# Kernel tuning notes

Hardware: AMD Instinct MI355X
Metric: run time of the kernel (lower is better)

The kernel has to match this reference:

```python
import jax, jax.numpy as jnp
import numpy as np

B, N, V = 1024, 256, 200


def setup_inputs() -> dict:
    key = jax.random.key(0)
    ks = jax.random.split(key, 24)
    merged = jax.random.normal(ks[0], (B, N, 15), dtype=jnp.float32)
    # active flag column in {0,1}; row 0 is the subject bus and is always active
    flag = (jax.random.uniform(ks[1], (B, N)) < 0.5).astype(jnp.float32)
    flag = flag.at[:, 0].set(1.0)
    merged = merged.at[:, :, 14].set(flag)
    a = jax.random.normal(ks[2], (B,), dtype=jnp.float32)
    w = lambda k, s: jax.random.normal(k, s, dtype=jnp.float32) * 0.05
    return dict(
        merged=merged, a=a,
        up_Wq=w(ks[3], (7, V)), up_Wk=w(ks[4], (14, V)), up_Wv=w(ks[5], (14, V)),
        dn_Wq=w(ks[6], (7, V)), dn_Wk=w(ks[7], (14, V)), dn_Wv=w(ks[8], (14, V)),
        pv_Wq=w(ks[9], (7, V)), pv_Wk=w(ks[10], (7, V)), pv_Wv=w(ks[11], (7, V)),
        t_W1=w(ks[12], (3, V, V)), t_b1=w(ks[13], (3, V)),
        t_W2=w(ks[14], (3, V, 1)), t_b2=w(ks[15], (3, 1)),
        e_W1=w(ks[16], (4, V)), e_b1=w(ks[17], (V,)),
        e_W2=w(ks[18], (V, V)), e_b2=w(ks[19], (V,)),
        e_W3=w(ks[20], (V, 1)), e_b3=w(ks[21], (1,)),
        gamma=jnp.ones((V,), jnp.float32), beta=jnp.zeros((V,), jnp.float32),
    )


def reference(merged, a, up_Wq, up_Wk, up_Wv, dn_Wq, dn_Wk, dn_Wv,
              pv_Wq, pv_Wk, pv_Wv, t_W1, t_b1, t_W2, t_b2,
              e_W1, e_b1, e_W2, e_b2, e_W3, e_b3, gamma, beta):
    v_dim = gamma.shape[0]
    scale = np.float32(1.0 / np.sqrt(v_dim))
    # merged_s[0, 6] = a  (subject bus action)
    merged = merged.at[:, 0, 6].set(a)
    # subtract subject bus id from id columns 0 and 7
    subj_id = merged[:, 0:1, 0]                       # [B,1]
    merged = merged.at[:, :, 0].add(-subj_id)
    merged = merged.at[:, :, 7].add(-subj_id)
    subj_loc = merged[:, 0:1, 2]                      # [B,1]
    flag = merged[:, :, 14]                           # [B,N]
    loc = merged[:, :, 2]                             # [B,N]
    up_mask = (loc < subj_loc) & (flag == 1.0)        # active upstream (excludes subject: loc==subj_loc)
    dn_mask = (loc > subj_loc) & (flag == 1.0)        # active downstream
    pv_mask = flag == 0.0                             # passive buses (row 0 is active by construction)
    ego = merged[:, 0, :7]                            # [B,7]
    f14 = merged[:, :, :14]                           # [B,N,14]
    f7 = merged[:, :, :7]                             # [B,N,7]

    def attend(Wq, Wk, Wv, feat, mask):
        # single-query cross attention: ego query vs ragged (masked) neighbor set
        q = ego @ Wq                                  # [B,V]
        k = jnp.einsum('bnf,fv->bnv', feat, Wk)
        v = jnp.einsum('bnf,fv->bnv', feat, Wv)
        s = jnp.einsum('bv,bnv->bn', q, k) * scale
        s = jnp.where(mask, s, jnp.float32(-1e9))
        out = jnp.einsum('bn,bnv->bv', jax.nn.softmax(s, axis=-1), v)
        # empty neighbor set -> zeros(v_dim) (compute_attention_target fallback)
        return jnp.where(mask.any(-1, keepdims=True), out, 0.0)

    u = attend(up_Wq, up_Wk, up_Wv, f14, up_mask)
    d = attend(dn_Wq, dn_Wk, dn_Wv, f14, dn_mask)
    p = attend(pv_Wq, pv_Wk, pv_Wv, f7, pv_mask)

    def bn(x):  # BatchNorm1d in training mode: batch statistics, biased var
        m = x.mean(0)
        var = x.var(0)
        return gamma * (x - m) * jax.lax.rsqrt(var + 1e-5) + beta

    t = jnp.stack([bn(u), bn(d), bn(p)], 0)           # [3,B,V]
    h = jax.nn.elu(jnp.einsum('kbv,kvw->kbw', t, t_W1) + t_b1[:, None, :])
    heads = jnp.einsum('kbw,kwo->kbo', h, t_W2) + t_b2[:, None, :]  # [3,B,1]
    ego_t = merged[:, 0, 3:7]                         # cols [3,4,5,6] = [hb,hf,occp,a]
    q1 = jax.nn.relu(ego_t @ e_W1 + e_b1)
    q1 = jax.nn.relu(q1 @ e_W2 + e_b2)
    Q1 = q1 @ e_W3 + e_b3                             # [B,1]
    G1 = Q1 + heads[0] + heads[1] + heads[2]
    return G1.reshape(-1, 1)
```

## Files before the change

kernel.cpp:

```cpp
#include <hip/hip_runtime.h>
#include <math.h>

#define BB 1024
#define NN 256
#define VV 200
#define BT 8
#define NSH 16

#define WS_M    0
#define WS_STAT 256
#define WS_X    19456

__global__ __launch_bounds__(256) void k_prep(const float* __restrict__ upWq, const float* __restrict__ upWk,
                                              const float* __restrict__ dnWq, const float* __restrict__ dnWk,
                                              const float* __restrict__ pvWq, const float* __restrict__ pvWk,
                                              float* __restrict__ ws, float* __restrict__ out) {
    __shared__ float wq[7 * VV];
    __shared__ float wk[14 * VV];
    int blk = blockIdx.x, tid = threadIdx.x;
    float* stat = ws + WS_STAT;
    for (int i = blk * 256 + tid; i < 2 * NSH * 600; i += 8 * 256) stat[i] = 0.f;
    for (int i = blk * 256 + tid; i < BB; i += 8 * 256) out[i] = 0.f;

    if (blk < 3) {
        const float* Wq = blk == 0 ? upWq : (blk == 1 ? dnWq : pvWq);
        const float* Wk = blk == 0 ? upWk : (blk == 1 ? dnWk : pvWk);
        int F = (blk == 2) ? 7 : 14;
        int off = blk == 0 ? 0 : (blk == 1 ? 98 : 196);
        for (int i = tid; i < 7 * VV; i += 256) wq[i] = Wq[i];
        for (int i = tid; i < F * VV; i += 256) wk[i] = Wk[i];
        __syncthreads();
        if (tid < 7 * F) {
            int i = tid / F, f = tid % F;
            float s = 0.f;
            for (int v = 0; v < VV; v++) s += wq[i * VV + v] * wk[f * VV + v];
            ws[WS_M + off + tid] = s;
        }
    }
}

__global__ __launch_bounds__(256) void k_attn(
    const float* __restrict__ merged, const float* __restrict__ a,
    const float* __restrict__ upWv, const float* __restrict__ dnWv, const float* __restrict__ pvWv,
    float* __restrict__ ws) {
    int b = blockIdx.x;
    int tid = threadIdx.x;
    int lane = tid & 63, wave = tid >> 6;

    __shared__ float sm[NN * 15];
    __shared__ float eMsh[35];
    __shared__ float psh[3 * NN];
    __shared__ float part[245];
    __shared__ float csh[35];
    __shared__ float wred[4][3];

    const float* gM = ws + WS_M;
    float* g_sum = ws + WS_STAT;
    float* g_ss  = ws + WS_STAT + NSH * 600;
    float* g_x   = ws + WS_X;

    const float4* g4 = (const float4*)(merged + (size_t)b * NN * 15);
    float4* s4p = (float4*)sm;
    for (int i = tid; i < NN * 15 / 4; i += 256) s4p[i] = g4[i];
    __syncthreads();

    float ab = a[b];
    float subj_id = sm[0];
    float subj_loc = sm[2];
    __syncthreads();

    sm[tid * 15 + 0] -= subj_id;
    sm[tid * 15 + 7] -= subj_id;
    if (tid == 0) sm[6] = ab;
    if (tid < 35) {
        int h = tid < 14 ? 0 : (tid < 28 ? 1 : 2);
        int f = tid - (h == 0 ? 0 : (h == 1 ? 14 : 28));
        int F = (h == 2) ? 7 : 14;
        const float* M = gM + (h == 0 ? 0 : (h == 1 ? 98 : 196));
        float e1 = sm[1], e2 = sm[2], e3 = sm[3], e4 = sm[4], e5 = sm[5];
        eMsh[tid] = e1 * M[1 * F + f] + e2 * M[2 * F + f] + e3 * M[3 * F + f] +
                    e4 * M[4 * F + f] + e5 * M[5 * F + f] + ab * M[6 * F + f];
    }
    __syncthreads();

    float feat[14];
#pragma unroll
    for (int f = 0; f < 14; f++) feat[f] = sm[tid * 15 + f];
    float flag = sm[tid * 15 + 14];
    float loc = feat[2];

    float s0 = 0.f, s1 = 0.f, s2 = 0.f;
#pragma unroll
    for (int f = 0; f < 14; f++) {
        s0 += eMsh[f] * feat[f];
        s1 += eMsh[14 + f] * feat[f];
    }
#pragma unroll
    for (int f = 0; f < 7; f++) s2 += eMsh[28 + f] * feat[f];

    const float scale = 7.0710678118654752e-2f;
    s0 = ((loc < subj_loc) && (flag == 1.f)) ? s0 * scale : -1e9f;
    s1 = ((loc > subj_loc) && (flag == 1.f)) ? s1 * scale : -1e9f;
    s2 = (flag == 0.f) ? s2 * scale : -1e9f;

    float m0 = s0, m1 = s1, m2 = s2;
#pragma unroll
    for (int off = 32; off; off >>= 1) {
        m0 = fmaxf(m0, __shfl_xor(m0, off));
        m1 = fmaxf(m1, __shfl_xor(m1, off));
        m2 = fmaxf(m2, __shfl_xor(m2, off));
    }
    if (lane == 0) { wred[wave][0] = m0; wred[wave][1] = m1; wred[wave][2] = m2; }
    __syncthreads();
    m0 = fmaxf(fmaxf(wred[0][0], wred[1][0]), fmaxf(wred[2][0], wred[3][0]));
    m1 = fmaxf(fmaxf(wred[0][1], wred[1][1]), fmaxf(wred[2][1], wred[3][1]));
    m2 = fmaxf(fmaxf(wred[0][2], wred[1][2]), fmaxf(wred[2][2], wred[3][2]));
    float e0 = expf(s0 - m0), e1 = expf(s1 - m1), e2 = expf(s2 - m2);
    float z0 = e0, z1 = e1, z2 = e2;
#pragma unroll
    for (int off = 32; off; off >>= 1) {
        z0 += __shfl_xor(z0, off);
        z1 += __shfl_xor(z1, off);
        z2 += __shfl_xor(z2, off);
    }
    __syncthreads();
    if (lane == 0) { wred[wave][0] = z0; wred[wave][1] = z1; wred[wave][2] = z2; }
    __syncthreads();
    z0 = wred[0][0] + wred[1][0] + wred[2][0] + wred[3][0];
    z1 = wred[0][1] + wred[1][1] + wred[2][1] + wred[3][1];
    z2 = wred[0][2] + wred[1][2] + wred[2][2] + wred[3][2];

    psh[0 * NN + tid] = e0 / z0;
    psh[1 * NN + tid] = e1 / z1;
    psh[2 * NN + tid] = e2 / z2;
    __syncthreads();

    if (tid < 245) {
        int d = tid / 7, j = tid % 7;
        int h = d < 14 ? 0 : (d < 28 ? 1 : 2);
        int f = d - (h == 0 ? 0 : (h == 1 ? 14 : 28));
        const float* p = psh + h * NN;
        float s = 0.f;
        for (int n = j; n < NN; n += 7) s += p[n] * sm[n * 15 + f];
        part[tid] = s;
    }
    __syncthreads();
    if (tid < 35) {
        float s = 0.f;
#pragma unroll
        for (int j = 0; j < 7; j++) s += part[tid * 7 + j];
        csh[tid] = s;
    }
    __syncthreads();

    if (tid < VV) {
        int shard = b & (NSH - 1);
        const float* Wvs[3] = {upWv, dnWv, pvWv};
        float mh[3] = {m0, m1, m2};
        const int coff[3] = {0, 14, 28};
        const int Fs[3] = {14, 14, 7};
#pragma unroll
        for (int h = 0; h < 3; h++) {
            const float* Wv = Wvs[h];
            const float* c = csh + coff[h];
            float val = 0.f;
            for (int f = 0; f < Fs[h]; f++) val += c[f] * Wv[f * VV + tid];
            if (mh[h] == -1e9f) val = 0.f;
            g_x[((size_t)h * BB + b) * VV + tid] = val;
            atomicAdd(&g_sum[shard * 600 + h * VV + tid], val);
            atomicAdd(&g_ss[shard * 600 + h * VV + tid], val * val);
        }
    }
}

__global__ __launch_bounds__(256) void k_final(const float* __restrict__ merged, const float* __restrict__ a,
                                               const float* __restrict__ tW1, const float* __restrict__ tb1,
                                               const float* __restrict__ tW2, const float* __restrict__ tb2,
                                               const float* __restrict__ eW1, const float* __restrict__ eb1,
                                               const float* __restrict__ eW2, const float* __restrict__ eb2,
                                               const float* __restrict__ eW3, const float* __restrict__ eb3,
                                               const float* __restrict__ gamma, const float* __restrict__ beta,
                                               const float* __restrict__ ws,
                                               float* __restrict__ out) {
    int tile = blockIdx.x >> 2;
    int q = blockIdx.x & 3;
    int b0 = tile * BT;
    int tid = threadIdx.x;
    int lane = tid & 63, wave = tid >> 6;
    int w = tid;

    __shared__ __align__(16) float tT[VV * BT];
    __shared__ float redsh[4 * BT];
    __shared__ float esh[BT][4];

    const float* g_sum = ws + WS_STAT;
    const float* g_ss  = ws + WS_STAT + NSH * 600;
    const float* g_x   = ws + WS_X;

    float fin[BT];
#pragma unroll
    for (int bb = 0; bb < BT; bb++) fin[bb] = 0.f;

    if (q < 3) {
        __shared__ float bnA[VV], bnB[VV];
        if (w < VV) {
            float S = 0.f, S2 = 0.f;
#pragma unroll
            for (int s = 0; s < NSH; s++) {
                S += g_sum[s * 600 + q * VV + w];
                S2 += g_ss[s * 600 + q * VV + w];
            }
            float m = S * (1.f / BB);
            float var = S2 * (1.f / BB) - m * m;
            float rstd = rsqrtf(var + 1e-5f);
            float gv = gamma[w];
            bnA[w] = gv * rstd;
            bnB[w] = beta[w] - gv * rstd * m;
        }
        __syncthreads();
        for (int idx = tid; idx < BT * VV; idx += 256) {
            int v = idx % VV, bb = idx / VV;
            float val = g_x[((size_t)q * BB + b0 + bb) * VV + v];
            tT[v * BT + bb] = bnA[v] * val + bnB[v];
        }
        __syncthreads();

        if (w < VV) {
            float acc[BT];
            float bias = tb1[q * VV + w];
#pragma unroll
            for (int bb = 0; bb < BT; bb++) acc[bb] = bias;
            const float* W1 = tW1 + (size_t)q * VV * VV + w;
            const float4* tT4 = (const float4*)tT;
#pragma unroll 8
            for (int v = 0; v < VV; v++) {
                float w1 = W1[(size_t)v * VV];
                float4 t0 = tT4[v * 2 + 0];
                float4 t1 = tT4[v * 2 + 1];
                acc[0] += t0.x * w1; acc[1] += t0.y * w1; acc[2] += t0.z * w1; acc[3] += t0.w * w1;
                acc[4] += t1.x * w1; acc[5] += t1.y * w1; acc[6] += t1.z * w1; acc[7] += t1.w * w1;
            }
            float w2 = tW2[q * VV + w];
#pragma unroll
            for (int bb = 0; bb < BT; bb++) {
                float h = acc[bb];
                h = h > 0.f ? h : expf(h) - 1.f;
                fin[bb] = h * w2;
            }
        }
    } else {
        if (tid < BT) {
            const float* mrow = merged + (size_t)(b0 + tid) * NN * 15;
            esh[tid][0] = mrow[3];
            esh[tid][1] = mrow[4];
            esh[tid][2] = mrow[5];
            esh[tid][3] = a[b0 + tid];
        }
        __syncthreads();
        if (w < VV) {
            float e0 = eW1[w], e1 = eW1[VV + w], e2 = eW1[2 * VV + w], e3 = eW1[3 * VV + w];
            float bias = eb1[w];
#pragma unroll
            for (int bb = 0; bb < BT; bb++) {
                float qv = bias + esh[bb][0] * e0 + esh[bb][1] * e1 + esh[bb][2] * e2 + esh[bb][3] * e3;
                tT[w * BT + bb] = fmaxf(qv, 0.f);
            }
        }
        __syncthreads();
        if (w < VV) {
            float acc[BT];
            float bias = eb2[w];
#pragma unroll
            for (int bb = 0; bb < BT; bb++) acc[bb] = bias;
            const float* W2 = eW2 + w;
            const float4* tT4 = (const float4*)tT;
#pragma unroll 8
            for (int v = 0; v < VV; v++) {
                float w2v = W2[(size_t)v * VV];
                float4 t0 = tT4[v * 2 + 0];
                float4 t1 = tT4[v * 2 + 1];
                acc[0] += t0.x * w2v; acc[1] += t0.y * w2v; acc[2] += t0.z * w2v; acc[3] += t0.w * w2v;
                acc[4] += t1.x * w2v; acc[5] += t1.y * w2v; acc[6] += t1.z * w2v; acc[7] += t1.w * w2v;
            }
            float w3 = eW3[w];
#pragma unroll
            for (int bb = 0; bb < BT; bb++) fin[bb] = fmaxf(acc[bb], 0.f) * w3;
        }
    }

#pragma unroll
    for (int bb = 0; bb < BT; bb++)
#pragma unroll
        for (int off = 32; off; off >>= 1) fin[bb] += __shfl_xor(fin[bb], off);
    if (lane == 0)
#pragma unroll
        for (int bb = 0; bb < BT; bb++) redsh[wave * BT + bb] = fin[bb];
    __syncthreads();
    if (tid < BT) {
        float tot = redsh[tid] + redsh[BT + tid] + redsh[2 * BT + tid] + redsh[3 * BT + tid];
        if (q == 3) tot += eb3[0] + tb2[0] + tb2[1] + tb2[2];
        atomicAdd(&out[b0 + tid], tot);
    }
}

extern "C" void kernel_launch(void* const* d_in, const int* in_sizes, int n_in,
                              void* d_out, int out_size, void* d_ws, size_t ws_size,
                              hipStream_t stream) {
    const float* merged = (const float*)d_in[0];
    const float* a      = (const float*)d_in[1];
    const float* upWq   = (const float*)d_in[2];
    const float* upWk   = (const float*)d_in[3];
    const float* upWv   = (const float*)d_in[4];
    const float* dnWq   = (const float*)d_in[5];
    const float* dnWk   = (const float*)d_in[6];
    const float* dnWv   = (const float*)d_in[7];
    const float* pvWq   = (const float*)d_in[8];
    const float* pvWk   = (const float*)d_in[9];
    const float* pvWv   = (const float*)d_in[10];
    const float* tW1    = (const float*)d_in[11];
    const float* tb1    = (const float*)d_in[12];
    const float* tW2    = (const float*)d_in[13];
    const float* tb2    = (const float*)d_in[14];
    const float* eW1    = (const float*)d_in[15];
    const float* eb1    = (const float*)d_in[16];
    const float* eW2    = (const float*)d_in[17];
    const float* eb2    = (const float*)d_in[18];
    const float* eW3    = (const float*)d_in[19];
    const float* eb3    = (const float*)d_in[20];
    const float* gamma  = (const float*)d_in[21];
    const float* beta   = (const float*)d_in[22];
    float* out = (float*)d_out;
    float* ws = (float*)d_ws;

    hipLaunchKernelGGL(k_prep, dim3(8), dim3(256), 0, stream, upWq, upWk, dnWq, dnWk, pvWq, pvWk, ws, out);
    hipLaunchKernelGGL(k_attn, dim3(BB), dim3(256), 0, stream, merged, a, upWv, dnWv, pvWv, ws);
    hipLaunchKernelGGL(k_final, dim3((BB / BT) * 4), dim3(256), 0, stream, merged, a,
                       tW1, tb1, tW2, tb2, eW1, eb1, eW2, eb2, eW3, eb3, gamma, beta, ws, out);
}
```

Before: 141.5 us.

## Process one batch row per wavefront in attention kernel with register-resident features

Restructures k_attn so each 64-lane wave handles one batch row, with four rows per block. Each lane holds four bus rows in registers, so block-wide barriers and the shared-memory staging of the merged tile are no longer needed. BatchNorm statistics are first accumulated in shared memory per block and then flushed to the global shards, which cuts global atomic traffic by four. Per-lane loads of 15 strided floats are uncoalesced, and the heavy register use under launch_bounds(256,1) may limit occupancy.

```diff
diff --git a/kernel.cpp b/kernel.cpp
--- a/kernel.cpp
+++ b/kernel.cpp
@@ -6,6 +6,7 @@
 #define VV 200
 #define BT 8
 #define NSH 16
+#define RPB 4
 
 #define WS_M    0
 #define WS_STAT 256
@@ -39,137 +40,161 @@
     }
 }
 
-__global__ __launch_bounds__(256) void k_attn(
+__global__ __launch_bounds__(256, 1) void k_attn(
     const float* __restrict__ merged, const float* __restrict__ a,
     const float* __restrict__ upWv, const float* __restrict__ dnWv, const float* __restrict__ pvWv,
     float* __restrict__ ws) {
-    int b = blockIdx.x;
     int tid = threadIdx.x;
     int lane = tid & 63, wave = tid >> 6;
-
-    __shared__ float sm[NN * 15];
-    __shared__ float eMsh[35];
-    __shared__ float psh[3 * NN];
-    __shared__ float part[245];
-    __shared__ float csh[35];
-    __shared__ float wred[4][3];
+    int b = blockIdx.x * RPB + wave;
+
+    __shared__ float eMsh[RPB][35];
+    __shared__ float csh[RPB][35];
+    __shared__ float partsh[RPB][64 * 37 + 1];
+    __shared__ float ssum[600], sss[600];
 
     const float* gM = ws + WS_M;
     float* g_sum = ws + WS_STAT;
     float* g_ss  = ws + WS_STAT + NSH * 600;
     float* g_x   = ws + WS_X;
 
-    const float4* g4 = (const float4*)(merged + (size_t)b * NN * 15);
-    float4* s4p = (float4*)sm;
-    for (int i = tid; i < NN * 15 / 4; i += 256) s4p[i] = g4[i];
+    for (int i = tid; i < 600; i += 256) { ssum[i] = 0.f; sss[i] = 0.f; }
     __syncthreads();
 
+    const float* row = merged + (size_t)b * (NN * 15);
     float ab = a[b];
-    float subj_id = sm[0];
-    float subj_loc = sm[2];
-    __syncthreads();
-
-    sm[tid * 15 + 0] -= subj_id;
-    sm[tid * 15 + 7] -= subj_id;
-    if (tid == 0) sm[6] = ab;
-    if (tid < 35) {
-        int h = tid < 14 ? 0 : (tid < 28 ? 1 : 2);
-        int f = tid - (h == 0 ? 0 : (h == 1 ? 14 : 28));
+    float subj_id  = row[0];
+    float e1v      = row[1];
+    float subj_loc = row[2];
+    float e3v = row[3], e4v = row[4], e5v = row[5];
+
+    float ft[4][15];
+#pragma unroll
+    for (int j = 0; j < 4; j++) {
+        const float* r = row + (lane + 64 * j) * 15;
+#pragma unroll
+        for (int c = 0; c < 15; c++) ft[j][c] = r[c];
+    }
+#pragma unroll
+    for (int j = 0; j < 4; j++) { ft[j][0] -= subj_id; ft[j][7] -= subj_id; }
+    if (lane == 0) ft[0][6] = ab;
+
+    if (lane < 35) {
+        int h = lane < 14 ? 0 : (lane < 28 ? 1 : 2);
+        int f = lane - (h == 0 ? 0 : (h == 1 ? 14 : 28));
         int F = (h == 2) ? 7 : 14;
         const float* M = gM + (h == 0 ? 0 : (h == 1 ? 98 : 196));
-        float e1 = sm[1], e2 = sm[2], e3 = sm[3], e4 = sm[4], e5 = sm[5];
-        eMsh[tid] = e1 * M[1 * F + f] + e2 * M[2 * F + f] + e3 * M[3 * F + f] +
-                    e4 * M[4 * F + f] + e5 * M[5 * F + f] + ab * M[6 * F + f];
-    }
-    __syncthreads();
-
-    float feat[14];
-#pragma unroll
-    for (int f = 0; f < 14; f++) feat[f] = sm[tid * 15 + f];
-    float flag = sm[tid * 15 + 14];
-    float loc = feat[2];
-
-    float s0 = 0.f, s1 = 0.f, s2 = 0.f;
-#pragma unroll
-    for (int f = 0; f < 14; f++) {
-        s0 += eMsh[f] * feat[f];
-        s1 += eMsh[14 + f] * feat[f];
-    }
-#pragma unroll
-    for (int f = 0; f < 7; f++) s2 += eMsh[28 + f] * feat[f];
+        eMsh[wave][f + (h == 0 ? 0 : (h == 1 ? 14 : 28))] =
+            e1v * M[1 * F + f] + subj_loc * M[2 * F + f] + e3v * M[3 * F + f] +
+            e4v * M[4 * F + f] + e5v * M[5 * F + f] + ab * M[6 * F + f];
+    }
+    asm volatile("s_waitcnt lgkmcnt(0)" ::: "memory");
+    __builtin_amdgcn_sched_barrier(0);
+
+    float eM[35];
+#pragma unroll
+    for (int f = 0; f < 35; f++) eM[f] = eMsh[wave][f];
 
     const float scale = 7.0710678118654752e-2f;
-    s0 = ((loc < subj_loc) && (flag == 1.f)) ? s0 * scale : -1e9f;
-    s1 = ((loc > subj_loc) && (flag == 1.f)) ? s1 * scale : -1e9f;
-    s2 = (flag == 0.f) ? s2 * scale : -1e9f;
-
-    float m0 = s0, m1 = s1, m2 = s2;
+    float s0[4], s1[4], s2[4];
+#pragma unroll
+    for (int j = 0; j < 4; j++) {
+        float a0 = 0.f, a1 = 0.f, a2 = 0.f;
+#pragma unroll
+        for (int f = 0; f < 14; f++) { a0 += eM[f] * ft[j][f]; a1 += eM[14 + f] * ft[j][f]; }
+#pragma unroll
+        for (int f = 0; f < 7; f++) a2 += eM[28 + f] * ft[j][f];
+        float loc = ft[j][2], flag = ft[j][14];
+        s0[j] = ((loc < subj_loc) && (flag == 1.f)) ? a0 * scale : -1e9f;
+        s1[j] = ((loc > subj_loc) && (flag == 1.f)) ? a1 * scale : -1e9f;
+        s2[j] = (flag == 0.f) ? a2 * scale : -1e9f;
+    }
+
+    float m0 = fmaxf(fmaxf(s0[0], s0[1]), fmaxf(s0[2], s0[3]));
+    float m1 = fmaxf(fmaxf(s1[0], s1[1]), fmaxf(s1[2], s1[3]));
+    float m2 = fmaxf(fmaxf(s2[0], s2[1]), fmaxf(s2[2], s2[3]));
 #pragma unroll
     for (int off = 32; off; off >>= 1) {
         m0 = fmaxf(m0, __shfl_xor(m0, off));
         m1 = fmaxf(m1, __shfl_xor(m1, off));
         m2 = fmaxf(m2, __shfl_xor(m2, off));
     }
-    if (lane == 0) { wred[wave][0] = m0; wred[wave][1] = m1; wred[wave][2] = m2; }
-    __syncthreads();
-    m0 = fmaxf(fmaxf(wred[0][0], wred[1][0]), fmaxf(wred[2][0], wred[3][0]));
-    m1 = fmaxf(fmaxf(wred[0][1], wred[1][1]), fmaxf(wred[2][1], wred[3][1]));
-    m2 = fmaxf(fmaxf(wred[0][2], wred[1][2]), fmaxf(wred[2][2], wred[3][2]));
-    float e0 = expf(s0 - m0), e1 = expf(s1 - m1), e2 = expf(s2 - m2);
-    float z0 = e0, z1 = e1, z2 = e2;
+    float p0[4], p1[4], p2[4];
+    float z0 = 0.f, z1 = 0.f, z2 = 0.f;
+#pragma unroll
+    for (int j = 0; j < 4; j++) {
+        p0[j] = expf(s0[j] - m0); z0 += p0[j];
+        p1[j] = expf(s1[j] - m1); z1 += p1[j];
+        p2[j] = expf(s2[j] - m2); z2 += p2[j];
+    }
 #pragma unroll
     for (int off = 32; off; off >>= 1) {
         z0 += __shfl_xor(z0, off);
         z1 += __shfl_xor(z1, off);
         z2 += __shfl_xor(z2, off);
     }
+    float iz0 = 1.f / z0, iz1 = 1.f / z1, iz2 = 1.f / z2;
+#pragma unroll
+    for (int j = 0; j < 4; j++) { p0[j] *= iz0; p1[j] *= iz1; p2[j] *= iz2; }
+
+    float pt[35];
+#pragma unroll
+    for (int f = 0; f < 14; f++)
+        pt[f] = p0[0] * ft[0][f] + p0[1] * ft[1][f] + p0[2] * ft[2][f] + p0[3] * ft[3][f];
+#pragma unroll
+    for (int f = 0; f < 14; f++)
+        pt[14 + f] = p1[0] * ft[0][f] + p1[1] * ft[1][f] + p1[2] * ft[2][f] + p1[3] * ft[3][f];
+#pragma unroll
+    for (int f = 0; f < 7; f++)
+        pt[28 + f] = p2[0] * ft[0][f] + p2[1] * ft[1][f] + p2[2] * ft[2][f] + p2[3] * ft[3][f];
+
+    {
+        float* pb = &partsh[wave][lane * 37];
+#pragma unroll
+        for (int d = 0; d < 35; d++) pb[d] = pt[d];
+    }
+    asm volatile("s_waitcnt lgkmcnt(0)" ::: "memory");
+    __builtin_amdgcn_sched_barrier(0);
+    if (lane < 35) {
+        const float* ps = &partsh[wave][lane];
+        float c = 0.f;
+#pragma unroll
+        for (int l = 0; l < 64; l++) c += ps[l * 37];
+        csh[wave][lane] = c;
+    }
+    asm volatile("s_waitcnt lgkmcnt(0)" ::: "memory");
+    __builtin_amdgcn_sched_barrier(0);
+
+    float cc[35];
+#pragma unroll
+    for (int d = 0; d < 35; d++) cc[d] = csh[wave][d];
+
+#pragma unroll
+    for (int vi = 0; vi < 4; vi++) {
+        int v = lane + 64 * vi;
+        if (v < VV) {
+            float v0 = 0.f, v1 = 0.f, v2 = 0.f;
+#pragma unroll
+            for (int f = 0; f < 14; f++) { v0 += cc[f] * upWv[f * VV + v]; v1 += cc[14 + f] * dnWv[f * VV + v]; }
+#pragma unroll
+            for (int f = 0; f < 7; f++) v2 += cc[28 + f] * pvWv[f * VV + v];
+            if (m0 == -1e9f) v0 = 0.f;
+            if (m1 == -1e9f) v1 = 0.f;
+            if (m2 == -1e9f) v2 = 0.f;
+            g_x[((size_t)0 * BB + b) * VV + v] = v0;
+            g_x[((size_t)1 * BB + b) * VV + v] = v1;
+            g_x[((size_t)2 * BB + b) * VV + v] = v2;
+            atomicAdd(&ssum[v], v0);            atomicAdd(&sss[v], v0 * v0);
+            atomicAdd(&ssum[VV + v], v1);       atomicAdd(&sss[VV + v], v1 * v1);
+            atomicAdd(&ssum[2 * VV + v], v2);   atomicAdd(&sss[2 * VV + v], v2 * v2);
+        }
+    }
+
     __syncthreads();
-    if (lane == 0) { wred[wave][0] = z0; wred[wave][1] = z1; wred[wave][2] = z2; }
-    __syncthreads();
-    z0 = wred[0][0] + wred[1][0] + wred[2][0] + wred[3][0];
-    z1 = wred[0][1] + wred[1][1] + wred[2][1] + wred[3][1];
-    z2 = wred[0][2] + wred[1][2] + wred[2][2] + wred[3][2];
-
-    psh[0 * NN + tid] = e0 / z0;
-    psh[1 * NN + tid] = e1 / z1;
-    psh[2 * NN + tid] = e2 / z2;
-    __syncthreads();
-
-    if (tid < 245) {
-        int d = tid / 7, j = tid % 7;
-        int h = d < 14 ? 0 : (d < 28 ? 1 : 2);
-        int f = d - (h == 0 ? 0 : (h == 1 ? 14 : 28));
-        const float* p = psh + h * NN;
-        float s = 0.f;
-        for (int n = j; n < NN; n += 7) s += p[n] * sm[n * 15 + f];
-        part[tid] = s;
-    }
-    __syncthreads();
-    if (tid < 35) {
-        float s = 0.f;
-#pragma unroll
-        for (int j = 0; j < 7; j++) s += part[tid * 7 + j];
-        csh[tid] = s;
-    }
-    __syncthreads();
-
-    if (tid < VV) {
-        int shard = b & (NSH - 1);
-        const float* Wvs[3] = {upWv, dnWv, pvWv};
-        float mh[3] = {m0, m1, m2};
-        const int coff[3] = {0, 14, 28};
-        const int Fs[3] = {14, 14, 7};
-#pragma unroll
-        for (int h = 0; h < 3; h++) {
-            const float* Wv = Wvs[h];
-            const float* c = csh + coff[h];
-            float val = 0.f;
-            for (int f = 0; f < Fs[h]; f++) val += c[f] * Wv[f * VV + tid];
-            if (mh[h] == -1e9f) val = 0.f;
-            g_x[((size_t)h * BB + b) * VV + tid] = val;
-            atomicAdd(&g_sum[shard * 600 + h * VV + tid], val);
-            atomicAdd(&g_ss[shard * 600 + h * VV + tid], val * val);
-        }
+    int shard = blockIdx.x & (NSH - 1);
+    for (int i = tid; i < 600; i += 256) {
+        atomicAdd(&g_sum[shard * 600 + i], ssum[i]);
+        atomicAdd(&g_ss[shard * 600 + i], sss[i]);
     }
 }
 
@@ -333,7 +358,7 @@
     float* ws = (float*)d_ws;
 
     hipLaunchKernelGGL(k_prep, dim3(8), dim3(256), 0, stream, upWq, upWk, dnWq, dnWk, pvWq, pvWk, ws, out);
-    hipLaunchKernelGGL(k_attn, dim3(BB), dim3(256), 0, stream, merged, a, upWv, dnWv, pvWv, ws);
+    hipLaunchKernelGGL(k_attn, dim3(BB / RPB), dim3(256), 0, stream, merged, a, upWv, dnWv, pvWv, ws);
     hipLaunchKernelGGL(k_final, dim3((BB / BT) * 4), dim3(256), 0, stream, merged, a,
                        tW1, tb1, tW2, tb2, eW1, eb1, eW2, eb2, eW3, eb3, gamma, beta, ws, out);
 }
```

Result: no change. 141.6 us (+0.0%).
